# Optimization experiments

Hardware: AMD Instinct MI355X
Metric: run time of the kernel (lower is better)

The kernel has to match this reference:

```python
import jax, jax.numpy as jnp
import numpy as np

N_NODES = 100000
N_EDGES = 1600000
IN_DIM, HID_DIM, OUT_DIM = 128, 128, 40
EPS = 1e-12


def setup_inputs() -> dict:
    key = jax.random.key(0)
    ks = jax.random.split(key, 7)
    x = jax.random.normal(ks[0], (N_NODES, IN_DIM), dtype=jnp.float32)
    edge_index = jax.random.randint(ks[1], (2, N_EDGES), 0, N_NODES, dtype=jnp.int64)
    s1 = 1.0 / np.sqrt(IN_DIM)
    s2 = 1.0 / np.sqrt(HID_DIM)
    return {
        "x": x,
        "edge_index": edge_index,
        "W1_l": jax.random.normal(ks[2], (HID_DIM, IN_DIM), dtype=jnp.float32) * s1,
        "b1": jnp.zeros((HID_DIM,), dtype=jnp.float32),
        "W1_r": jax.random.normal(ks[3], (HID_DIM, IN_DIM), dtype=jnp.float32) * s1,
        "W2_l": jax.random.normal(ks[4], (OUT_DIM, HID_DIM), dtype=jnp.float32) * s2,
        "b2": jnp.zeros((OUT_DIM,), dtype=jnp.float32),
        "W2_r": jax.random.normal(ks[5], (OUT_DIM, HID_DIM), dtype=jnp.float32) * s2,
    }


def _mean_aggregate(x, src, dst, deg_inv):
    # gather source features, scatter-sum into destination nodes, divide by degree
    summed = jax.ops.segment_sum(x[src], dst, num_segments=N_NODES)  # [N, d]
    return summed * deg_inv[:, None]


def _sage_conv(x, src, dst, deg_inv, W_l, b_l, W_r):
    # PyG SAGEConv(mean, normalize=True): lin_l(mean(x_j)) + lin_r(x_i), then L2-normalize
    agg = _mean_aggregate(x, src, dst, deg_inv)
    out = agg @ W_l.T + b_l + x @ W_r.T
    norm = jnp.sqrt(jnp.sum(out * out, axis=-1, keepdims=True))
    return out / jnp.maximum(norm, EPS)


def reference(x, edge_index, W1_l, b1, W1_r, W2_l, b2, W2_r):
    src, dst = edge_index[0], edge_index[1]
    deg = jax.ops.segment_sum(jnp.ones((src.shape[0],), dtype=x.dtype), dst,
                              num_segments=N_NODES)
    deg_inv = 1.0 / jnp.maximum(deg, 1.0)

    h = _sage_conv(x, src, dst, deg_inv, W1_l, b1, W1_r)
    h = jax.nn.relu(h)  # dropout = identity (deterministic reference)
    h = _sage_conv(h, src, dst, deg_inv, W2_l, b2, W2_r)
    h = jax.nn.relu(h)
    return jax.nn.log_softmax(h, axis=-1)
```

## Files before the change

### kernel.cpp

```cpp
#include <hip/hip_runtime.h>
#include <hip/hip_bf16.h>

#define N_NODES 100000
#define N_EDGES 1600000
#define IN_DIM 128
#define HID_DIM 128
#define OUT_DIM 40

#define BSHIFT 9
#define NBUCK 196
#define CHUNK 4096
#define NCHUNK ((N_EDGES + CHUNK - 1) / CHUNK)

typedef __attribute__((ext_vector_type(8))) short short8;
typedef __attribute__((ext_vector_type(4))) float float4v;
typedef __attribute__((ext_vector_type(2))) float f32x2;
typedef __attribute__((ext_vector_type(2))) unsigned int u32x2;
typedef __attribute__((ext_vector_type(4))) unsigned int u32x4;

typedef unsigned char u8;
typedef unsigned short u16;
typedef unsigned int u32;
typedef unsigned long long u64;

__device__ __forceinline__ float bflo(u32 v) { union { u32 u; float f; } c; c.u = v << 16; return c.f; }
__device__ __forceinline__ float bfhi(u32 v) { union { u32 u; float f; } c; c.u = v & 0xffff0000u; return c.f; }
__device__ __forceinline__ u16 f2bf(float f) {
    union { float f; u32 u; } c; c.f = f;
    u32 r = c.u + 0x7fffu + ((c.u >> 16) & 1u);
    return (u16)(r >> 16);
}
__device__ __forceinline__ u32 pk(float lo, float hi) {
    return ((u32)f2bf(hi) << 16) | (u32)f2bf(lo);
}

__device__ __forceinline__ u32 f2fp8(float f) {
    union { float f; u32 u; } c; c.f = f;
    u32 s = (c.u >> 24) & 0x80u;
    u32 a = c.u & 0x7fffffffu;
    u32 code;
    if (a >= 0x3C800000u) {
        if (a > 0x43E00000u) a = 0x43E00000u;
        u32 r = a + 0x0007FFFFu + ((a >> 20) & 1u);
        code = (((r >> 23) - 120u) << 3) | ((r >> 20) & 7u);
        if (code > 0x7Eu) code = 0x7Eu;
    } else {
        union { u32 u; float f; } d; d.u = a;
        code = (u32)(int)rintf(d.f * 512.0f);
    }
    return s | code;
}


#define XBLKS ((N_NODES * IN_DIM / 4 + 255) / 256)
#define WTRIP1 2048
#define WTRIP2 768
#define WBLKS 22

__global__ __launch_bounds__(256) void k_cvtall(
    const float* __restrict__ x, u16* __restrict__ xb, u32* __restrict__ xb8,
    const float* __restrict__ w1l, const float* __restrict__ w1r,
    const float* __restrict__ w2l, const float* __restrict__ w2r,
    u16* __restrict__ w1lf, u16* __restrict__ w1rf,
    u16* __restrict__ w2lf, u16* __restrict__ w2rf,
    const int* __restrict__ idx, int* __restrict__ bucket_size) {
    __shared__ int cnt[NBUCK];
    int b = blockIdx.x;
    if (b < XBLKS) {
        int i = b * 256 + threadIdx.x;
        if (i < N_NODES * IN_DIM / 4) {
            float4v v = reinterpret_cast<const float4v*>(x)[i];
            u32x2 o;
            o.x = pk(v.x, v.y);
            o.y = pk(v.z, v.w);
            reinterpret_cast<u32x2*>(xb)[i] = o;
            xb8[i] = f2fp8(v.x) | (f2fp8(v.y) << 8) | (f2fp8(v.z) << 16) | (f2fp8(v.w) << 24);
        }
        return;
    }
    if (b < XBLKS + WBLKS) {
        int i = (b - XBLKS) * 256 + threadIdx.x;
        const float* s; u16* d; int t; int rows;
        if (i < WTRIP1)            { s = w1l; d = w1lf; t = i;                 rows = HID_DIM; }
        else if (i < 2*WTRIP1)     { s = w1r; d = w1rf; t = i - WTRIP1;        rows = HID_DIM; }
        else if (i < 2*WTRIP1+WTRIP2)   { s = w2l; d = w2lf; t = i - 2*WTRIP1; rows = OUT_DIM; }
        else if (i < 2*WTRIP1+2*WTRIP2) { s = w2r; d = w2rf; t = i - 2*WTRIP1-WTRIP2; rows = OUT_DIM; }
        else return;
        int lane = t & 63;
        int ks = (t >> 6) & 3;
        int ct = t >> 8;
        int row = ct * 16 + (lane & 15);
        int col = ks * 32 + (lane >> 4) * 8;
        u32x4 o;
        if (row < rows) {
            const float* sp = s + row * 128 + col;
            float4v v0 = *reinterpret_cast<const float4v*>(sp);
            float4v v1 = *reinterpret_cast<const float4v*>(sp + 4);
            o.x = pk(v0.x, v0.y); o.y = pk(v0.z, v0.w);
            o.z = pk(v1.x, v1.y); o.w = pk(v1.z, v1.w);
        } else { o.x = 0; o.y = 0; o.z = 0; o.w = 0; }
        reinterpret_cast<u32x4*>(d)[t] = o;
        return;
    }
    int t = threadIdx.x;
    for (int i = t; i < NBUCK; i += 256) cnt[i] = 0;
    __syncthreads();
    int base = (b - XBLKS - WBLKS) * CHUNK;
    int n = min(CHUNK, N_EDGES - base);
    for (int i = t; i < n; i += 256)
        atomicAdd(&cnt[idx[N_EDGES + base + i] >> BSHIFT], 1);
    __syncthreads();
    for (int i = t; i < NBUCK; i += 256)
        if (cnt[i]) atomicAdd(&bucket_size[i], cnt[i]);
}


__global__ __launch_bounds__(1024) void k_bscatter(const int* __restrict__ idx,
                                                   const int* __restrict__ bucket_size,
                                                   int* __restrict__ bucket_cur,
                                                   u64* __restrict__ rec) {
    __shared__ int cnt[NBUCK], gbase[NBUCK];
    __shared__ int sa[256], sb[256];
    int t = threadIdx.x;
    const int nt = 1024;
    for (int i = t; i < NBUCK; i += nt) cnt[i] = 0;
    __syncthreads();
    int base = blockIdx.x * CHUNK;
    int n = min(CHUNK, N_EDGES - base);
    int eb[4], eq[4];
    u64 er[4];
    #pragma unroll
    for (int k = 0; k < 4; ++k) {
        int i = t + k * nt;
        if (i < n) {
            int srcv = idx[base + i];
            int dstv = idx[N_EDGES + base + i];
            int b = dstv >> BSHIFT;
            eb[k] = b;
            eq[k] = atomicAdd(&cnt[b], 1);
            er[k] = ((u64)(u32)dstv << 32) | (u32)srcv;
        }
    }
    int myv = 0;
    if (t < 256) {
        myv = (t < NBUCK) ? bucket_size[t] : 0;
        sa[t] = myv;
    }
    __syncthreads();
    int *s = sa, *d = sb;
    for (int dd = 1; dd < 256; dd <<= 1) {
        if (t < 256) d[t] = s[t] + ((t >= dd) ? s[t - dd] : 0);
        __syncthreads();
        int* tm = s; s = d; d = tm;
    }
    if (t < NBUCK) {
        int v = cnt[t];
        gbase[t] = v ? (s[t] - myv) + atomicAdd(&bucket_cur[t], v) : 0;
    }
    __syncthreads();
    #pragma unroll
    for (int k = 0; k < 4; ++k) {
        int i = t + k * nt;
        if (i < n) rec[gbase[eb[k]] + eq[k]] = er[k];
    }
}

__global__ __launch_bounds__(1024) void k_bfill(const u64* __restrict__ rec,
                                                const int* __restrict__ bucket_size,
                                                int* __restrict__ row_start,
                                                int* __restrict__ csr) {
    __shared__ int deg[512], cur[512];
    __shared__ int sa[512], sb[512];
    int t = threadIdx.x;
    int nt = blockDim.x;
    int b = blockIdx.x;
    int node0 = b << BSHIFT;
    int nn = min(512, N_NODES - node0);
    int esz = bucket_size[b];
    if (t < 256) sa[t] = (t < NBUCK) ? bucket_size[t] : 0;
    __syncthreads();
    {
        int *s = sa, *d = sb;
        for (int dd = 1; dd < 256; dd <<= 1) {
            if (t < 256) d[t] = s[t] + ((t >= dd) ? s[t - dd] : 0);
            __syncthreads();
            int* tm = s; s = d; d = tm;
        }
        if (t == 0) cur[0] = s[b] - esz;
    }
    __syncthreads();
    int ebase = cur[0];
    __syncthreads();
    for (int i = t; i < 512; i += nt) deg[i] = 0;
    __syncthreads();
    for (int i = t; i < esz; i += nt)
        atomicAdd(&deg[((int)(rec[ebase + i] >> 32)) & 511], 1);
    __syncthreads();
    for (int i = t; i < 512; i += nt) sa[i] = deg[i];
    __syncthreads();
    int *s = sa, *d = sb;
    for (int dd = 1; dd < 512; dd <<= 1) {
        for (int i = t; i < 512; i += nt) d[i] = s[i] + ((i >= dd) ? s[i - dd] : 0);
        __syncthreads();
        int* tm = s; s = d; d = tm;
    }
    for (int i = t; i < 512; i += nt) {
        int excl = s[i] - deg[i];
        cur[i] = excl;
        if (i < nn) row_start[node0 + i] = ebase + excl;
    }
    if (b == NBUCK - 1 && t == 0) row_start[N_NODES] = N_EDGES;
    __syncthreads();
    for (int i = t; i < esz; i += nt) {
        u64 r = rec[ebase + i];
        int dl = ((int)(r >> 32)) & 511;
        int p = atomicAdd(&cur[dl], 1);
        csr[ebase + p] = (int)(r & 0xffffffffu);
    }
}


__global__ void k_agg(const u32x2* __restrict__ fp,
                      const int* __restrict__ csr,
                      const int* __restrict__ row_start,
                      u16* __restrict__ agg) {
    int n = blockIdx.x * 4 + (threadIdx.x >> 6);
    int lane = threadIdx.x & 63;
    if (n >= N_NODES) return;
    int s = row_start[n];
    int e = row_start[n + 1];
    int g = lane >> 4;
    int li = lane & 15;
    f32x2 ac0 = {0.f, 0.f}, ac1 = {0.f, 0.f}, ac2 = {0.f, 0.f}, ac3 = {0.f, 0.f};
#define ACC8(v) do { \
        ac0 += __builtin_amdgcn_cvt_pk_f32_fp8((v).x, false); \
        ac1 += __builtin_amdgcn_cvt_pk_f32_fp8((v).x, true);  \
        ac2 += __builtin_amdgcn_cvt_pk_f32_fp8((v).y, false); \
        ac3 += __builtin_amdgcn_cvt_pk_f32_fp8((v).y, true);  \
    } while (0)
    int p = s;
    int i0 = 0, i1 = 0;
    if (p + 8 <= e) { i0 = csr[p + g]; i1 = csr[p + 4 + g]; }
    while (p + 8 <= e) {
        u32x2 v0 = fp[i0 * 16 + li];
        u32x2 v1 = fp[i1 * 16 + li];
        p += 8;
        if (p + 8 <= e) { i0 = csr[p + g]; i1 = csr[p + 4 + g]; }
        ACC8(v0);
        ACC8(v1);
    }
    if (p + g < e) { u32x2 v = fp[csr[p + g] * 16 + li]; ACC8(v); }
    if (p + 4 + g < e) { u32x2 v = fp[csr[p + 4 + g] * 16 + li]; ACC8(v); }
#undef ACC8
    float a0 = ac0.x, a1 = ac0.y, a2 = ac1.x, a3 = ac1.y;
    float a4 = ac2.x, a5 = ac2.y, a6 = ac3.x, a7 = ac3.y;
    a0 += __shfl_xor(a0, 16); a0 += __shfl_xor(a0, 32);
    a1 += __shfl_xor(a1, 16); a1 += __shfl_xor(a1, 32);
    a2 += __shfl_xor(a2, 16); a2 += __shfl_xor(a2, 32);
    a3 += __shfl_xor(a3, 16); a3 += __shfl_xor(a3, 32);
    a4 += __shfl_xor(a4, 16); a4 += __shfl_xor(a4, 32);
    a5 += __shfl_xor(a5, 16); a5 += __shfl_xor(a5, 32);
    a6 += __shfl_xor(a6, 16); a6 += __shfl_xor(a6, 32);
    a7 += __shfl_xor(a7, 16); a7 += __shfl_xor(a7, 32);
    if (g == 0) {
        float sc = 1.0f / (float)max(e - s, 1);
        u32x4 o;
        o.x = pk(a0 * sc, a1 * sc);
        o.y = pk(a2 * sc, a3 * sc);
        o.z = pk(a4 * sc, a5 * sc);
        o.w = pk(a6 * sc, a7 * sc);
        *reinterpret_cast<u32x4*>(agg + n * 128 + li * 8) = o;
    }
}


__global__ __launch_bounds__(256) void k_dense1(
    const u16* __restrict__ agg, const u16* __restrict__ x,
    const u16* __restrict__ W1lf, const u16* __restrict__ W1rf,
    const float* __restrict__ b1, u16* __restrict__ h) {
    __shared__ short8 wsh[2][WTRIP1];
    int t = threadIdx.x;
    int wave = t >> 6;
    int lane = t & 63;
    int nb = blockIdx.x * 64 + wave * 16;
    int q = lane >> 4;
    int m = lane & 15;
    int arow = nb + m;
    if (arow >= N_NODES) arow = N_NODES - 1;

    short8 afr[8];
    #pragma unroll
    for (int ks = 0; ks < 4; ++ks) {
        afr[ks]     = *reinterpret_cast<const short8*>(agg + arow * 128 + ks * 32 + q * 8);
        afr[4 + ks] = *reinterpret_cast<const short8*>(x   + arow * 128 + ks * 32 + q * 8);
    }
    const short8* g0 = reinterpret_cast<const short8*>(W1lf);
    const short8* g1 = reinterpret_cast<const short8*>(W1rf);
    #pragma unroll
    for (int k = 0; k < 8; ++k) {
        wsh[0][t + k * 256] = g0[t + k * 256];
        wsh[1][t + k * 256] = g1[t + k * 256];
    }
    __syncthreads();

    float4v acc[8];
    #pragma unroll
    for (int ct = 0; ct < 8; ++ct) acc[ct] = (float4v){0.f, 0.f, 0.f, 0.f};

    #pragma unroll
    for (int half = 0; half < 2; ++half)
        #pragma unroll
        for (int ks = 0; ks < 4; ++ks) {
            short8 a = afr[half * 4 + ks];
            #pragma unroll
            for (int ct = 0; ct < 8; ++ct) {
                short8 b = wsh[half][(ct * 4 + ks) * 64 + lane];
                acc[ct] = __builtin_amdgcn_mfma_f32_16x16x32_bf16(a, b, acc[ct], 0, 0, 0);
            }
        }

    float bias[8];
    #pragma unroll
    for (int ct = 0; ct < 8; ++ct) bias[ct] = b1[ct * 16 + m];

    float nsq[4] = { 0.f, 0.f, 0.f, 0.f };
    #pragma unroll
    for (int ct = 0; ct < 8; ++ct)
        #pragma unroll
        for (int r = 0; r < 4; ++r) {
            float v = acc[ct][r] + bias[ct];
            acc[ct][r] = v;
            nsq[r] += v * v;
        }
    #pragma unroll
    for (int r = 0; r < 4; ++r) {
        float tt = nsq[r];
        tt += __shfl_xor(tt, 1);
        tt += __shfl_xor(tt, 2);
        tt += __shfl_xor(tt, 4);
        tt += __shfl_xor(tt, 8);
        nsq[r] = 1.0f / fmaxf(sqrtf(tt), 1e-12f);
    }
    #pragma unroll
    for (int r = 0; r < 4; ++r) {
        int node = nb + q * 4 + r;
        if (node < N_NODES) {
            #pragma unroll
            for (int ct = 0; ct < 8; ++ct) {
                float v = fmaxf(acc[ct][r] * nsq[r], 0.0f);
                h[node * 128 + ct * 16 + m] = f2bf(v);
            }
        }
    }
}


__global__ __launch_bounds__(256) void k_dense2a(
    const u16* __restrict__ h,
    const u16* __restrict__ W2lf, const u16* __restrict__ W2rf,
    u8* __restrict__ y2, u16* __restrict__ z) {
    __shared__ short8 wsh[2][WTRIP2];
    int t = threadIdx.x;
    int wave = t >> 6;
    int lane = t & 63;
    int nb = blockIdx.x * 64 + wave * 16;
    int q = lane >> 4;
    int m = lane & 15;
    int arow = nb + m;
    if (arow >= N_NODES) arow = N_NODES - 1;

    short8 afr[4];
    #pragma unroll
    for (int ks = 0; ks < 4; ++ks)
        afr[ks] = *reinterpret_cast<const short8*>(h + arow * 128 + ks * 32 + q * 8);
    const short8* g0 = reinterpret_cast<const short8*>(W2lf);
    const short8* g1 = reinterpret_cast<const short8*>(W2rf);
    #pragma unroll
    for (int k = 0; k < 3; ++k) {
        wsh[0][t + k * 256] = g0[t + k * 256];
        wsh[1][t + k * 256] = g1[t + k * 256];
    }
    __syncthreads();

    float4v accl[3], accr[3];
    #pragma unroll
    for (int ct = 0; ct < 3; ++ct) {
        accl[ct] = (float4v){0.f, 0.f, 0.f, 0.f};
        accr[ct] = (float4v){0.f, 0.f, 0.f, 0.f};
    }
    #pragma unroll
    for (int ks = 0; ks < 4; ++ks) {
        short8 a = afr[ks];
        #pragma unroll
        for (int ct = 0; ct < 3; ++ct) {
            accl[ct] = __builtin_amdgcn_mfma_f32_16x16x32_bf16(a, wsh[0][(ct * 4 + ks) * 64 + lane], accl[ct], 0, 0, 0);
            accr[ct] = __builtin_amdgcn_mfma_f32_16x16x32_bf16(a, wsh[1][(ct * 4 + ks) * 64 + lane], accr[ct], 0, 0, 0);
        }
    }
    #pragma unroll
    for (int r = 0; r < 4; ++r) {
        int node = nb + q * 4 + r;
        if (node < N_NODES) {
            #pragma unroll
            for (int ct = 0; ct < 3; ++ct) {
                int col = ct * 16 + m;
                y2[node * 64 + col] = (u8)f2fp8(accl[ct][r] * 64.0f);
                z[node * 48 + col]  = f2bf(accr[ct][r]);
            }
            y2[node * 64 + 48 + m] = 0;
        }
    }
}


__global__ void k_agg2(const u32x2* __restrict__ fp,
                       const int* __restrict__ csr,
                       const int* __restrict__ row_start,
                       const u16* __restrict__ z,
                       const float* __restrict__ b2,
                       float* __restrict__ out) {
    int n = blockIdx.x * 4 + (threadIdx.x >> 6);
    int lane = threadIdx.x & 63;
    if (n >= N_NODES) return;
    int s = row_start[n];
    int e = row_start[n + 1];
    int g = lane >> 3;
    int li = lane & 7;
    f32x2 ac0 = {0.f, 0.f}, ac1 = {0.f, 0.f}, ac2 = {0.f, 0.f}, ac3 = {0.f, 0.f};
#define ACC8(v) do { \
        ac0 += __builtin_amdgcn_cvt_pk_f32_fp8((v).x, false); \
        ac1 += __builtin_amdgcn_cvt_pk_f32_fp8((v).x, true);  \
        ac2 += __builtin_amdgcn_cvt_pk_f32_fp8((v).y, false); \
        ac3 += __builtin_amdgcn_cvt_pk_f32_fp8((v).y, true);  \
    } while (0)
    int p = s;
    int i0 = 0, i1 = 0;
    if (p + 16 <= e) { i0 = csr[p + g]; i1 = csr[p + 8 + g]; }
    while (p + 16 <= e) {
        u32x2 v0 = fp[i0 * 8 + li];
        u32x2 v1 = fp[i1 * 8 + li];
        p += 16;
        if (p + 16 <= e) { i0 = csr[p + g]; i1 = csr[p + 8 + g]; }
        ACC8(v0);
        ACC8(v1);
    }
    if (p + g < e) { u32x2 v = fp[csr[p + g] * 8 + li]; ACC8(v); }
    if (p + 8 + g < e) { u32x2 v = fp[csr[p + 8 + g] * 8 + li]; ACC8(v); }
#undef ACC8
    float a[8] = { ac0.x, ac0.y, ac1.x, ac1.y, ac2.x, ac2.y, ac3.x, ac3.y };
    #pragma unroll
    for (int j = 0; j < 8; ++j) {
        a[j] += __shfl_xor(a[j], 8);
        a[j] += __shfl_xor(a[j], 16);
        a[j] += __shfl_xor(a[j], 32);
    }

    float sc = 1.0f / (64.0f * (float)max(e - s, 1));
    float v[8];
    if (li < 5) {
        u32x4 zv = *reinterpret_cast<const u32x4*>(z + n * 48 + li * 8);
        float4v bv0 = *reinterpret_cast<const float4v*>(b2 + li * 8);
        float4v bv1 = *reinterpret_cast<const float4v*>(b2 + li * 8 + 4);
        v[0] = a[0] * sc + bflo(zv.x) + bv0.x;
        v[1] = a[1] * sc + bfhi(zv.x) + bv0.y;
        v[2] = a[2] * sc + bflo(zv.y) + bv0.z;
        v[3] = a[3] * sc + bfhi(zv.y) + bv0.w;
        v[4] = a[4] * sc + bflo(zv.z) + bv1.x;
        v[5] = a[5] * sc + bfhi(zv.z) + bv1.y;
        v[6] = a[6] * sc + bflo(zv.w) + bv1.z;
        v[7] = a[7] * sc + bfhi(zv.w) + bv1.w;
    } else {
        #pragma unroll
        for (int j = 0; j < 8; ++j) v[j] = 0.f;
    }
    float nsq = 0.f;
    #pragma unroll
    for (int j = 0; j < 8; ++j) nsq += v[j] * v[j];
    nsq += __shfl_xor(nsq, 1);
    nsq += __shfl_xor(nsq, 2);
    nsq += __shfl_xor(nsq, 4);
    float rn = 1.0f / fmaxf(sqrtf(nsq), 1e-12f);
    float mv = 0.f;
    #pragma unroll
    for (int j = 0; j < 8; ++j) {
        v[j] = fmaxf(v[j] * rn, 0.f);
        mv = fmaxf(mv, v[j]);
    }
    mv = fmaxf(mv, __shfl_xor(mv, 1));
    mv = fmaxf(mv, __shfl_xor(mv, 2));
    mv = fmaxf(mv, __shfl_xor(mv, 4));
    float se = 0.f;
    if (li < 5) {
        #pragma unroll
        for (int j = 0; j < 8; ++j) se += __expf(v[j] - mv);
    }
    se += __shfl_xor(se, 1);
    se += __shfl_xor(se, 2);
    se += __shfl_xor(se, 4);
    float lse = __logf(se);
    if (g == 0 && li < 5) {
        float4v o0 = { v[0] - mv - lse, v[1] - mv - lse, v[2] - mv - lse, v[3] - mv - lse };
        float4v o1 = { v[4] - mv - lse, v[5] - mv - lse, v[6] - mv - lse, v[7] - mv - lse };
        *reinterpret_cast<float4v*>(out + n * OUT_DIM + li * 8) = o0;
        *reinterpret_cast<float4v*>(out + n * OUT_DIM + li * 8 + 4) = o1;
    }
}


extern "C" void kernel_launch(void* const* d_in, const int* in_sizes, int n_in,
                              void* d_out, int out_size, void* d_ws, size_t ws_size,
                              hipStream_t stream) {
    const float* x   = (const float*)d_in[0];
    const int*   idx = (const int*)d_in[1];
    const float* W1l = (const float*)d_in[2];
    const float* b1  = (const float*)d_in[3];
    const float* W1r = (const float*)d_in[4];
    const float* W2l = (const float*)d_in[5];
    const float* b2  = (const float*)d_in[6];
    const float* W2r = (const float*)d_in[7];
    float* out = (float*)d_out;

    char* ws = (char*)d_ws;
    int*   bucket_size = (int*)(ws + 0);
    int*   bucket_cur  = (int*)(ws + 1024);
    int*   row_start   = (int*)(ws + 16384);
    int*   csr         = (int*)(ws + 1216384);
    u16*   xb          = (u16*)(ws + 7616512);
    u8*    y2          = (u8*)(ws + 7616512);
    u16*   z           = (u16*)(ws + 20416512);
    u16*   agg         = (u16*)(ws + 33216512);
    u64*   rec         = (u64*)(ws + 58816512);
    u32*   xb8         = (u32*)(ws + 71616512);
    u16*   h           = (u16*)(ws + 58816512);
    u16*   W1lf        = (u16*)(ws + 84416512);
    u16*   W1rf        = (u16*)(ws + 84449280);
    u16*   W2lf        = (u16*)(ws + 84482048);
    u16*   W2rf        = (u16*)(ws + 84494336);

    hipMemsetAsync(ws, 0, 1808, stream);

    k_cvtall<<<XBLKS + WBLKS + NCHUNK, 256, 0, stream>>>(
        x, xb, xb8, W1l, W1r, W2l, W2r, W1lf, W1rf, W2lf, W2rf, idx, bucket_size);

    k_bscatter<<<NCHUNK, 1024, 0, stream>>>(idx, bucket_size, bucket_cur, rec);
    k_bfill<<<NBUCK, 1024, 0, stream>>>(rec, bucket_size, row_start, csr);

    k_agg<<<N_NODES / 4, 256, 0, stream>>>((const u32x2*)xb8, csr, row_start, agg);
    k_dense1<<<(N_NODES + 63) / 64, 256, 0, stream>>>(agg, xb, W1lf, W1rf, b1, h);
    k_dense2a<<<(N_NODES + 63) / 64, 256, 0, stream>>>(h, W2lf, W2rf, y2, z);
    k_agg2<<<N_NODES / 4, 256, 0, stream>>>((const u32x2*)y2, csr, row_start, z, b2, out);
}
```

Baseline: 283.0 us.

## Map one node per lane group in aggregation kernels instead of per wave

Both gather-aggregation kernels now assign one destination node to each 16-lane group (layer 1) or 8-lane group (layer 2), so a wave covers 4 or 8 nodes. Previously a whole wave worked on one node with edges split across groups. Each group walks its node's edge list two at a time, which removes the cross-group shuffle reduction and the single-group writeback. Grids shrink to match. In exchange, per-node edge loops get longer and serial, and lanes in a wave can diverge when node degrees differ.

```diff
diff --git a/kernel.cpp b/kernel.cpp
--- a/kernel.cpp
+++ b/kernel.cpp
@@ -224,13 +224,13 @@
                       const int* __restrict__ csr,
                       const int* __restrict__ row_start,
                       u16* __restrict__ agg) {
-    int n = blockIdx.x * 4 + (threadIdx.x >> 6);
     int lane = threadIdx.x & 63;
-    if (n >= N_NODES) return;
+    int wave = threadIdx.x >> 6;
+    int sub = lane >> 4;
+    int li = lane & 15;
+    int n = blockIdx.x * 16 + wave * 4 + sub;
     int s = row_start[n];
     int e = row_start[n + 1];
-    int g = lane >> 4;
-    int li = lane & 15;
     f32x2 ac0 = {0.f, 0.f}, ac1 = {0.f, 0.f}, ac2 = {0.f, 0.f}, ac3 = {0.f, 0.f};
 #define ACC8(v) do { \
         ac0 += __builtin_amdgcn_cvt_pk_f32_fp8((v).x, false); \
@@ -240,37 +240,24 @@
     } while (0)
     int p = s;
     int i0 = 0, i1 = 0;
-    if (p + 8 <= e) { i0 = csr[p + g]; i1 = csr[p + 4 + g]; }
-    while (p + 8 <= e) {
+    if (p + 2 <= e) { i0 = csr[p]; i1 = csr[p + 1]; }
+    while (p + 2 <= e) {
         u32x2 v0 = fp[i0 * 16 + li];
         u32x2 v1 = fp[i1 * 16 + li];
-        p += 8;
-        if (p + 8 <= e) { i0 = csr[p + g]; i1 = csr[p + 4 + g]; }
+        p += 2;
+        if (p + 2 <= e) { i0 = csr[p]; i1 = csr[p + 1]; }
         ACC8(v0);
         ACC8(v1);
     }
-    if (p + g < e) { u32x2 v = fp[csr[p + g] * 16 + li]; ACC8(v); }
-    if (p + 4 + g < e) { u32x2 v = fp[csr[p + 4 + g] * 16 + li]; ACC8(v); }
+    if (p < e) { u32x2 v = fp[csr[p] * 16 + li]; ACC8(v); }
 #undef ACC8
-    float a0 = ac0.x, a1 = ac0.y, a2 = ac1.x, a3 = ac1.y;
-    float a4 = ac2.x, a5 = ac2.y, a6 = ac3.x, a7 = ac3.y;
-    a0 += __shfl_xor(a0, 16); a0 += __shfl_xor(a0, 32);
-    a1 += __shfl_xor(a1, 16); a1 += __shfl_xor(a1, 32);
-    a2 += __shfl_xor(a2, 16); a2 += __shfl_xor(a2, 32);
-    a3 += __shfl_xor(a3, 16); a3 += __shfl_xor(a3, 32);
-    a4 += __shfl_xor(a4, 16); a4 += __shfl_xor(a4, 32);
-    a5 += __shfl_xor(a5, 16); a5 += __shfl_xor(a5, 32);
-    a6 += __shfl_xor(a6, 16); a6 += __shfl_xor(a6, 32);
-    a7 += __shfl_xor(a7, 16); a7 += __shfl_xor(a7, 32);
-    if (g == 0) {
-        float sc = 1.0f / (float)max(e - s, 1);
-        u32x4 o;
-        o.x = pk(a0 * sc, a1 * sc);
-        o.y = pk(a2 * sc, a3 * sc);
-        o.z = pk(a4 * sc, a5 * sc);
-        o.w = pk(a6 * sc, a7 * sc);
-        *reinterpret_cast<u32x4*>(agg + n * 128 + li * 8) = o;
-    }
+    float sc = 1.0f / (float)max(e - s, 1);
+    u32x4 o;
+    o.x = pk(ac0.x * sc, ac0.y * sc);
+    o.y = pk(ac1.x * sc, ac1.y * sc);
+    o.z = pk(ac2.x * sc, ac2.y * sc);
+    o.w = pk(ac3.x * sc, ac3.y * sc);
+    *reinterpret_cast<u32x4*>(agg + n * 128 + li * 8) = o;
 }
 
 
@@ -419,13 +406,13 @@
                        const u16* __restrict__ z,
                        const float* __restrict__ b2,
                        float* __restrict__ out) {
-    int n = blockIdx.x * 4 + (threadIdx.x >> 6);
     int lane = threadIdx.x & 63;
-    if (n >= N_NODES) return;
+    int wave = threadIdx.x >> 6;
+    int sub = lane >> 3;
+    int li = lane & 7;
+    int n = blockIdx.x * 32 + wave * 8 + sub;
     int s = row_start[n];
     int e = row_start[n + 1];
-    int g = lane >> 3;
-    int li = lane & 7;
     f32x2 ac0 = {0.f, 0.f}, ac1 = {0.f, 0.f}, ac2 = {0.f, 0.f}, ac3 = {0.f, 0.f};
 #define ACC8(v) do { \
         ac0 += __builtin_amdgcn_cvt_pk_f32_fp8((v).x, false); \
@@ -435,25 +422,18 @@
     } while (0)
     int p = s;
     int i0 = 0, i1 = 0;
-    if (p + 16 <= e) { i0 = csr[p + g]; i1 = csr[p + 8 + g]; }
-    while (p + 16 <= e) {
+    if (p + 2 <= e) { i0 = csr[p]; i1 = csr[p + 1]; }
+    while (p + 2 <= e) {
         u32x2 v0 = fp[i0 * 8 + li];
         u32x2 v1 = fp[i1 * 8 + li];
-        p += 16;
-        if (p + 16 <= e) { i0 = csr[p + g]; i1 = csr[p + 8 + g]; }
+        p += 2;
+        if (p + 2 <= e) { i0 = csr[p]; i1 = csr[p + 1]; }
         ACC8(v0);
         ACC8(v1);
     }
-    if (p + g < e) { u32x2 v = fp[csr[p + g] * 8 + li]; ACC8(v); }
-    if (p + 8 + g < e) { u32x2 v = fp[csr[p + 8 + g] * 8 + li]; ACC8(v); }
+    if (p < e) { u32x2 v = fp[csr[p] * 8 + li]; ACC8(v); }
 #undef ACC8
     float a[8] = { ac0.x, ac0.y, ac1.x, ac1.y, ac2.x, ac2.y, ac3.x, ac3.y };
-    #pragma unroll
-    for (int j = 0; j < 8; ++j) {
-        a[j] += __shfl_xor(a[j], 8);
-        a[j] += __shfl_xor(a[j], 16);
-        a[j] += __shfl_xor(a[j], 32);
-    }
 
     float sc = 1.0f / (64.0f * (float)max(e - s, 1));
     float v[8];
@@ -498,7 +478,7 @@
     se += __shfl_xor(se, 2);
     se += __shfl_xor(se, 4);
     float lse = __logf(se);
-    if (g == 0 && li < 5) {
+    if (li < 5) {
         float4v o0 = { v[0] - mv - lse, v[1] - mv - lse, v[2] - mv - lse, v[3] - mv - lse };
         float4v o1 = { v[4] - mv - lse, v[5] - mv - lse, v[6] - mv - lse, v[7] - mv - lse };
         *reinterpret_cast<float4v*>(out + n * OUT_DIM + li * 8) = o0;
@@ -545,8 +525,8 @@
     k_bscatter<<<NCHUNK, 1024, 0, stream>>>(idx, bucket_size, bucket_cur, rec);
     k_bfill<<<NBUCK, 1024, 0, stream>>>(rec, bucket_size, row_start, csr);
 
-    k_agg<<<N_NODES / 4, 256, 0, stream>>>((const u32x2*)xb8, csr, row_start, agg);
+    k_agg<<<N_NODES / 16, 256, 0, stream>>>((const u32x2*)xb8, csr, row_start, agg);
     k_dense1<<<(N_NODES + 63) / 64, 256, 0, stream>>>(agg, xb, W1lf, W1rf, b1, h);
     k_dense2a<<<(N_NODES + 63) / 64, 256, 0, stream>>>(h, W2lf, W2rf, y2, z);
-    k_agg2<<<N_NODES / 4, 256, 0, stream>>>((const u32x2*)y2, csr, row_start, z, b2, out);
-}
+    k_agg2<<<N_NODES / 32, 256, 0, stream>>>((const u32x2*)y2, csr, row_start, z, b2, out);
+}
```

Result: faster. 249.0 us (-12.0%).
